# Kernel tuning notes

Hardware: AMD Instinct MI355X
Metric: run time of the kernel (lower is better)

Reference implementation:

```python
import jax, jax.numpy as jnp
import numpy as np

B, N, PAST = 2, 1024, 1024
DIM, HEADS, DH = 2048, 16, 128
INNER = HEADS * DH
LN_EPS = 1e-5
ROPE_THETA = 10000.0


def setup_inputs() -> dict:
    key = jax.random.key(0)
    k0, k1, k2, k3, k4 = jax.random.split(key, 5)
    x = jax.random.normal(k0, (B, N, DIM), dtype=jnp.float32)
    past_k = jax.random.normal(k1, (B, HEADS, PAST, DH), dtype=jnp.float32)
    past_v = jax.random.normal(k2, (B, HEADS, PAST, DH), dtype=jnp.float32)
    # causal mask with KV-cache offset: query i sits at global pos PAST+i,
    # mask (True = blocked) keys at positions j > PAST+i
    kv = PAST + N
    q_pos = PAST + jnp.arange(N)
    k_pos = jnp.arange(kv)
    mask = jnp.broadcast_to((k_pos[None, :] > q_pos[:, None])[None, None], (B, 1, N, kv))
    w_qkv = jax.random.normal(k3, (DIM, 3 * INNER), dtype=jnp.float32) * (DIM ** -0.5)
    w_out = jax.random.normal(k4, (INNER, DIM), dtype=jnp.float32) * (INNER ** -0.5)
    ln_g = jnp.ones((DIM,), dtype=jnp.float32)
    ln_b = jnp.zeros((DIM,), dtype=jnp.float32)
    return {"x": x, "past_k": past_k, "past_v": past_v, "mask": mask,
            "w_qkv": w_qkv, "w_out": w_out, "ln_g": ln_g, "ln_b": ln_b}


def _layernorm(x, g, b):
    mu = jnp.mean(x, axis=-1, keepdims=True)
    var = jnp.mean((x - mu) ** 2, axis=-1, keepdims=True)
    return (x - mu) * jax.lax.rsqrt(var + LN_EPS) * g + b


def _rope(t, pos):
    # interleaved rotary (lucidrains rotary-embedding-torch convention)
    inv_freq = 1.0 / (ROPE_THETA ** (jnp.arange(0, DH, 2, dtype=jnp.float32) / DH))
    freqs = pos.astype(jnp.float32)[:, None] * inv_freq[None, :]   # [n, DH/2]
    freqs = jnp.repeat(freqs, 2, axis=-1)                          # [n, DH]
    cos = jnp.cos(freqs).astype(t.dtype)
    sin = jnp.sin(freqs).astype(t.dtype)
    t2 = t.reshape(*t.shape[:-1], DH // 2, 2)
    rot = jnp.stack((-t2[..., 1], t2[..., 0]), axis=-1).reshape(t.shape)
    return t * cos + rot * sin


def reference(x, past_k, past_v, mask, w_qkv, w_out, ln_g, ln_b):
    b, n, _ = x.shape
    xn = _layernorm(x, ln_g, ln_b)
    qkv = xn @ w_qkv                                               # [b, n, 3*INNER]
    q, k, v = jnp.split(qkv, 3, axis=-1)
    to_heads = lambda t: t.reshape(b, n, HEADS, DH).transpose(0, 2, 1, 3)  # b h n d
    q, k, v = to_heads(q), to_heads(k), to_heads(v)
    k = jnp.concatenate((past_k, k), axis=2)                       # [b, h, kv, d]
    v = jnp.concatenate((past_v, v), axis=2)
    kv_len = k.shape[2]
    q = _rope(q, jnp.arange(n) + (kv_len - n))
    k = _rope(k, jnp.arange(kv_len))
    scale = DH ** -0.5
    dots = jnp.einsum('bhnd,bhmd->bhnm', q, k) * scale             # [b, h, n, kv]
    dots = jnp.where(mask, -jnp.inf, dots)
    attn = jax.nn.softmax(dots, axis=-1)
    out = jnp.einsum('bhnm,bhmd->bhnd', attn, v)                   # [b, h, n, d]
    out = out.transpose(0, 2, 1, 3).reshape(b, n, INNER)
    return out @ w_out, k, v
```

## Files before the change

kernel.cpp:

```cpp
#include <hip/hip_runtime.h>
#include <hip/hip_bf16.h>
#include <math.h>

#define BB    2
#define NN    1024
#define PAST  1024
#define KVL   2048
#define DIM   2048
#define HEADS 16
#define DH    128
#define INNER 2048
#define NQKV  6144
#define TOK   2048
#define LN_EPS 1e-5f

typedef __attribute__((ext_vector_type(8))) short   short8;
typedef __attribute__((ext_vector_type(4))) float   f32x4;
typedef __attribute__((ext_vector_type(8))) unsigned short us8;
typedef __attribute__((ext_vector_type(4))) unsigned short us4;
typedef unsigned short us;

__device__ __forceinline__ float bfbits2f(us u) {
    return __uint_as_float(((unsigned int)u) << 16);
}
__device__ __forceinline__ us f2bfb(float f) {
    union { __hip_bfloat16 h; us u; } cv;
    cv.h = __float2bfloat16(f);
    return cv.u;
}
__device__ __forceinline__ us8 pack8u(float4 a, float4 b) {
    us8 r;
    r[0] = f2bfb(a.x); r[1] = f2bfb(a.y); r[2] = f2bfb(a.z); r[3] = f2bfb(a.w);
    r[4] = f2bfb(b.x); r[5] = f2bfb(b.y); r[6] = f2bfb(b.z); r[7] = f2bfb(b.w);
    return r;
}

__device__ __forceinline__ void gload_lds16(const void* gsrc, void* ldst) {
    __builtin_amdgcn_global_load_lds(
        (const __attribute__((address_space(1))) void*)gsrc,
        (__attribute__((address_space(3))) void*)ldst, 16, 0, 0);
}

__global__ __launch_bounds__(256) void transp_kernel(
    const float* __restrict__ src, us* __restrict__ dst, int R, int C)
{
    const int c0 = blockIdx.x * 64;
    const int r0 = blockIdx.y * 64;
    const int tid = threadIdx.x;

    __shared__ us T[64][68];

    #pragma unroll
    for (int e = 0; e < 4; e++) {
        int idx = tid + e * 256;
        int jr  = idx >> 4;
        int c4  = (idx & 15) * 4;
        float4 v = *reinterpret_cast<const float4*>(
            src + (size_t)(r0 + jr) * C + c0 + c4);
        us4 w;
        w[0] = f2bfb(v.x); w[1] = f2bfb(v.y); w[2] = f2bfb(v.z); w[3] = f2bfb(v.w);
        *reinterpret_cast<us4*>(&T[jr][c4]) = w;
    }
    __syncthreads();

    #pragma unroll
    for (int e = 0; e < 4; e++) {
        int idx = tid + e * 256;
        int d   = idx >> 4;
        int k4  = (idx & 15) * 4;
        us4 w;
        w[0] = T[k4 + 0][d];
        w[1] = T[k4 + 1][d];
        w[2] = T[k4 + 2][d];
        w[3] = T[k4 + 3][d];
        *reinterpret_cast<us4*>(dst + (size_t)(c0 + d) * R + r0 + k4) = w;
    }
}

__global__ __launch_bounds__(256) void ln_kernel(
    const float* __restrict__ x, const float* __restrict__ g,
    const float* __restrict__ b, us* __restrict__ xn)
{
    const int t   = blockIdx.x;
    const int tid = threadIdx.x;
    const size_t base = (size_t)t * DIM;

    float4 p0 = reinterpret_cast<const float4*>(x + base)[tid * 2 + 0];
    float4 p1 = reinterpret_cast<const float4*>(x + base)[tid * 2 + 1];
    float v[8] = {p0.x, p0.y, p0.z, p0.w, p1.x, p1.y, p1.z, p1.w};

    float s1 = 0.f, s2 = 0.f;
    #pragma unroll
    for (int i = 0; i < 8; i++) { s1 += v[i]; s2 += v[i] * v[i]; }

    #pragma unroll
    for (int off = 32; off; off >>= 1) {
        s1 += __shfl_xor(s1, off);
        s2 += __shfl_xor(s2, off);
    }
    __shared__ float red1[4], red2[4];
    if ((tid & 63) == 0) { red1[tid >> 6] = s1; red2[tid >> 6] = s2; }
    __syncthreads();
    float S1 = red1[0] + red1[1] + red1[2] + red1[3];
    float S2 = red2[0] + red2[1] + red2[2] + red2[3];
    const float inv = 1.0f / (float)DIM;
    float mu  = S1 * inv;
    float var = S2 * inv - mu * mu;
    float rstd = rsqrtf(var + LN_EPS);

    const int d0 = tid * 8;
    float4 oa, ob;
    oa.x = (v[0] - mu) * rstd * g[d0 + 0] + b[d0 + 0];
    oa.y = (v[1] - mu) * rstd * g[d0 + 1] + b[d0 + 1];
    oa.z = (v[2] - mu) * rstd * g[d0 + 2] + b[d0 + 2];
    oa.w = (v[3] - mu) * rstd * g[d0 + 3] + b[d0 + 3];
    ob.x = (v[4] - mu) * rstd * g[d0 + 4] + b[d0 + 4];
    ob.y = (v[5] - mu) * rstd * g[d0 + 5] + b[d0 + 5];
    ob.z = (v[6] - mu) * rstd * g[d0 + 6] + b[d0 + 6];
    ob.w = (v[7] - mu) * rstd * g[d0 + 7] + b[d0 + 7];

    *reinterpret_cast<us8*>(xn + base + d0) = pack8u(oa, ob);
}

template<bool OUT_BF16>
__global__ __launch_bounds__(256) void gemm_bt_kernel(
    const us* __restrict__ A, const us* __restrict__ Bt,
    void* __restrict__ Cout, int M, int N, int K)
{
    __shared__ us As[2][128 * 32];
    __shared__ us Bs[2][128 * 32];

    const int tid  = threadIdx.x;
    const int wave = tid >> 6, lane = tid & 63;
    const int quad = lane >> 4, l16 = lane & 15;
    const int wm = wave & 1, wn = wave >> 1;
    const int m0 = blockIdx.y * 128, n0 = blockIdx.x * 128;

    f32x4 acc[4][4];
    #pragma unroll
    for (int i = 0; i < 4; i++)
        #pragma unroll
        for (int j = 0; j < 4; j++)
            #pragma unroll
            for (int r = 0; r < 4; r++) acc[i][j][r] = 0.f;

    const int s_row = tid >> 2;
    const int s_c8  = (tid & 3) * 8;

    auto stage = [&](int k0, int buf) {
        #pragma unroll
        for (int e = 0; e < 2; e++) {
            gload_lds16(A  + (size_t)(m0 + e * 64 + s_row) * K + k0 + s_c8,
                        (char*)&As[buf][0] + (e * 256 + tid) * 16);
            gload_lds16(Bt + (size_t)(n0 + e * 64 + s_row) * K + k0 + s_c8,
                        (char*)&Bs[buf][0] + (e * 256 + tid) * 16);
        }
    };

    stage(0, 0);
    __syncthreads();

    int buf = 0;
    for (int k0 = 0; k0 < K; k0 += 32) {
        if (k0 + 32 < K) stage(k0 + 32, buf ^ 1);

        short8 af[4], bf[4];
        #pragma unroll
        for (int mi = 0; mi < 4; mi++)
            af[mi] = *reinterpret_cast<const short8*>(
                &As[buf][(wm * 64 + mi * 16 + l16) * 32 + quad * 8]);
        #pragma unroll
        for (int ni = 0; ni < 4; ni++)
            bf[ni] = *reinterpret_cast<const short8*>(
                &Bs[buf][(wn * 64 + ni * 16 + l16) * 32 + quad * 8]);

        __builtin_amdgcn_s_setprio(1);
        #pragma unroll
        for (int mi = 0; mi < 4; mi++)
            #pragma unroll
            for (int ni = 0; ni < 4; ni++)
                acc[mi][ni] = __builtin_amdgcn_mfma_f32_16x16x32_bf16(
                    af[mi], bf[ni], acc[mi][ni], 0, 0, 0);
        __builtin_amdgcn_s_setprio(0);

        __syncthreads();
        buf ^= 1;
    }

    #pragma unroll
    for (int mi = 0; mi < 4; mi++) {
        #pragma unroll
        for (int r = 0; r < 4; r++) {
            size_t row = (size_t)(m0 + wm * 64 + mi * 16 + quad * 4 + r);
            #pragma unroll
            for (int ni = 0; ni < 4; ni++) {
                size_t col = n0 + wn * 64 + ni * 16 + l16;
                if (OUT_BF16)
                    ((us*)Cout)[row * N + col] = f2bfb(acc[mi][ni][r]);
                else
                    ((float*)Cout)[row * N + col] = acc[mi][ni][r];
            }
        }
    }
}

__global__ __launch_bounds__(256) void rope_kernel(
    const float* __restrict__ past_k, const float* __restrict__ past_v,
    us* __restrict__ qkv, float* __restrict__ out_k, float* __restrict__ out_v,
    us* __restrict__ Kbf)
{
    const int tid  = threadIdx.x;
    const int pid  = blockIdx.x * 4 + (tid >> 6);
    const int lane = tid & 63;

    const int b   = pid / (HEADS * KVL);
    const int rem = pid - b * (HEADS * KVL);
    const int h   = rem / KVL;
    const int pos = rem - h * KVL;

    const float invf = exp2f((float)lane * (-13.287712379549449f / 64.0f));
    float sn, cs;
    sincosf((float)pos * invf, &sn, &cs);

    const size_t obase = ((size_t)(b * HEADS + h) * KVL + pos) * DH + 2 * lane;

    float k0, k1;
    if (pos < PAST) {
        const size_t pbase = ((size_t)(b * HEADS + h) * PAST + pos) * DH + 2 * lane;
        k0 = past_k[pbase];
        k1 = past_k[pbase + 1];
    } else {
        const int t = b * NN + (pos - PAST);
        const us* qp = qkv + (size_t)t * NQKV + INNER + h * DH + 2 * lane;
        k0 = bfbits2f(qp[0]); k1 = bfbits2f(qp[1]);
    }
    float kr0 = k0 * cs - k1 * sn;
    float kr1 = k1 * cs + k0 * sn;
    out_k[obase]     = kr0;
    out_k[obase + 1] = kr1;
    Kbf[obase]       = f2bfb(kr0);
    Kbf[obase + 1]   = f2bfb(kr1);

    if (pos < PAST) {
        const size_t pbase = ((size_t)(b * HEADS + h) * PAST + pos) * DH + 2 * lane;
        out_v[obase]     = past_v[pbase];
        out_v[obase + 1] = past_v[pbase + 1];
    } else {
        const int t = b * NN + (pos - PAST);
        const us* vp = qkv + (size_t)t * NQKV + 2 * INNER + h * DH + 2 * lane;
        out_v[obase]     = bfbits2f(vp[0]);
        out_v[obase + 1] = bfbits2f(vp[1]);
    }

    if (pos >= PAST) {
        const int t = b * NN + (pos - PAST);
        us* qq = qkv + (size_t)t * NQKV + h * DH + 2 * lane;
        float q0 = bfbits2f(qq[0]), q1 = bfbits2f(qq[1]);
        qq[0] = f2bfb(q0 * cs - q1 * sn);
        qq[1] = f2bfb(q1 * cs + q0 * sn);
    }
}

__global__ __launch_bounds__(256) void vtrans_kernel(
    const float* __restrict__ Vc, us* __restrict__ Vtg)
{
    const int jb = blockIdx.x;
    const int db = blockIdx.y;
    const int bh = blockIdx.z;
    const int tid = threadIdx.x;

    __shared__ us T[64][68];

    const float* src = Vc + ((size_t)bh * KVL + jb * 64) * DH + db * 64;
    #pragma unroll
    for (int e = 0; e < 4; e++) {
        int idx = tid + e * 256;
        int jr  = idx >> 4;
        int c4  = (idx & 15) * 4;
        float4 v = *reinterpret_cast<const float4*>(src + (size_t)jr * DH + c4);
        us4 w;
        w[0] = f2bfb(v.x); w[1] = f2bfb(v.y); w[2] = f2bfb(v.z); w[3] = f2bfb(v.w);
        *reinterpret_cast<us4*>(&T[jr][c4]) = w;
    }
    __syncthreads();

    us* dst = Vtg + ((size_t)bh * DH + db * 64) * KVL + jb * 64;
    #pragma unroll
    for (int e = 0; e < 4; e++) {
        int idx = tid + e * 256;
        int d   = idx >> 4;
        int k4  = (idx & 15) * 4;
        us4 w;
        w[0] = T[k4 + 0][d];
        w[1] = T[k4 + 1][d];
        w[2] = T[k4 + 2][d];
        w[3] = T[k4 + 3][d];
        *reinterpret_cast<us4*>(dst + (size_t)d * KVL + k4) = w;
    }
}

__global__ __launch_bounds__(512) void attn_mfma_kernel(
    const us* __restrict__ qkv,
    const us* __restrict__ Kbf,
    const us* __restrict__ Vtg,
    us* __restrict__ Ao)
{
    const int tid  = threadIdx.x;
    const int wave = tid >> 6;
    const int lane = tid & 63;
    const int quad = lane >> 4;
    const int l16  = lane & 15;

    const int flat = blockIdx.x;
    const int s    = flat >> 3;
    const int g    = (flat & 7) + 8 * (s & 3);
    const int p    = s >> 2;
    const int h    = g & 15;
    const int b    = g >> 4;
    const int qtile = (wave < 4) ? p : (15 - p);
    const int nch   = 32 - p;
    const int mynch = (wave < 4) ? (17 + p) : (32 - p);

    __shared__ us Ks[2][64 * 128];
    __shared__ us Vt[2][128 * 64];
    __shared__ us Pb[8][16 * 64];

    short8 qf[4];
    {
        const int qrow = qtile * 64 + (wave & 3) * 16 + l16;
        const us* qp = qkv + (size_t)(b * NN + qrow) * NQKV + h * DH;
        #pragma unroll
        for (int ks = 0; ks < 4; ks++)
            qf[ks] = *reinterpret_cast<const short8*>(qp + ks * 32 + quad * 8);
    }

    f32x4 Oacc[8];
    #pragma unroll
    for (int t = 0; t < 8; t++)
        #pragma unroll
        for (int r = 0; r < 4; r++) Oacc[t][r] = 0.f;
    float m_run  = -INFINITY;
    float l_part = 0.f;

    const us* kptr = Kbf + (size_t)(b * HEADS + h) * KVL * DH;
    const us* vtb  = Vtg + (size_t)(b * HEADS + h) * DH * KVL;
    const float scale = 0.08838834764831845f;
    const float THRU  = 90.50966799f;
    const int qg  = PAST + qtile * 64 + (wave & 3) * 16 + l16;
    const int swz = (l16 & 7) << 4;
    char* pbb = (char*)&Pb[wave][0];

    auto stage = [&](int j0, int buf) {
        #pragma unroll
        for (int e = 0; e < 2; e++) {
            int phys = (e * 512 + tid) * 16;
            int row  = phys >> 8;
            int col  = (phys & 255) ^ ((row & 7) << 4);
            gload_lds16((const char*)(kptr + (size_t)(j0 + row) * DH) + col,
                        (char*)&Ks[buf][0] + phys);
        }
        #pragma unroll
        for (int e = 0; e < 2; e++) {
            int phys = (e * 512 + tid) * 16;
            int row  = phys >> 7;
            int col  = (phys & 127) ^ ((row & 7) << 4);
            gload_lds16((const char*)(vtb + (size_t)row * KVL) + j0 * 2 + col,
                        (char*)&Vt[buf][0] + phys);
        }
    };

    stage(0, 0);
    __syncthreads();

    int cur = 0;
    for (int c = 0; c < nch; c++) {
        const int j0 = c * 64;
        if (c + 1 < nch) stage(j0 + 64, cur ^ 1);

        if (c < mynch) {
            f32x4 S[4];
            #pragma unroll
            for (int t = 0; t < 4; t++)
                #pragma unroll
                for (int r = 0; r < 4; r++) S[t][r] = 0.f;
            __builtin_amdgcn_s_setprio(1);
            #pragma unroll
            for (int ks = 0; ks < 4; ks++) {
                #pragma unroll
                for (int t = 0; t < 4; t++) {
                    int row  = t * 16 + l16;
                    int colb = ks * 64 + quad * 16;
                    const char* kp = (const char*)&Ks[cur][0] +
                                    row * 256 + (colb ^ ((row & 7) << 4));
                    short8 kb = *reinterpret_cast<const short8*>(kp);
                    S[t] = __builtin_amdgcn_mfma_f32_16x16x32_bf16(kb, qf[ks], S[t], 0, 0, 0);
                }
            }
            __builtin_amdgcn_s_setprio(0);

            const int rel = qg - j0;
            float mx = -INFINITY;
            #pragma unroll
            for (int t = 0; t < 4; t++) {
                #pragma unroll
                for (int r = 0; r < 4; r++) {
                    int koff = t * 16 + quad * 4 + r;
                    S[t][r] = (koff <= rel) ? S[t][r] : -INFINITY;
                    mx = fmaxf(mx, S[t][r]);
                }
            }
            mx = fmaxf(mx, __shfl_xor(mx, 16));
            mx = fmaxf(mx, __shfl_xor(mx, 32));

            float alpha = 1.f;
            if (__any(mx > m_run + THRU)) {
                float nm = fmaxf(m_run, mx);
                alpha = __expf((m_run - nm) * scale);
                m_run = nm;
                float al[4];
                #pragma unroll
                for (int r = 0; r < 4; r++) al[r] = __shfl(alpha, quad * 4 + r);
                #pragma unroll
                for (int t2 = 0; t2 < 8; t2++) {
                    Oacc[t2][0] *= al[0]; Oacc[t2][1] *= al[1];
                    Oacc[t2][2] *= al[2]; Oacc[t2][3] *= al[3];
                }
            }

            const float nmk = -m_run * scale;
            float rs = 0.f;
            #pragma unroll
            for (int t = 0; t < 4; t++) {
                us4 w;
                #pragma unroll
                for (int r = 0; r < 4; r++) {
                    float pv = __expf(fmaf(S[t][r], scale, nmk));
                    rs += pv;
                    w[r] = f2bfb(pv);
                }
                *reinterpret_cast<us4*>(pbb + l16 * 128 +
                                        ((t * 32 + quad * 8) ^ swz)) = w;
            }
            l_part = l_part * alpha + rs;

            asm volatile("s_waitcnt lgkmcnt(0)" ::: "memory");
            __builtin_amdgcn_sched_barrier(0);

            __builtin_amdgcn_s_setprio(1);
            #pragma unroll
            for (int kh = 0; kh < 2; kh++) {
                short8 pa = *reinterpret_cast<const short8*>(
                    pbb + l16 * 128 + ((kh * 64 + quad * 16) ^ swz));
                #pragma unroll
                for (int t2 = 0; t2 < 8; t2++) {
                    int row  = t2 * 16 + l16;
                    int colb = kh * 64 + quad * 16;
                    const char* vp = (const char*)&Vt[cur][0] +
                                    row * 128 + (colb ^ ((row & 7) << 4));
                    short8 vb = *reinterpret_cast<const short8*>(vp);
                    Oacc[t2] = __builtin_amdgcn_mfma_f32_16x16x32_bf16(pa, vb, Oacc[t2], 0, 0, 0);
                }
            }
            __builtin_amdgcn_s_setprio(0);
        }

        __syncthreads();
        cur ^= 1;
    }

    l_part += __shfl_xor(l_part, 16);
    l_part += __shfl_xor(l_part, 32);
    float invl[4];
    #pragma unroll
    for (int r = 0; r < 4; r++)
        invl[r] = 1.f / __shfl(l_part, quad * 4 + r);

    const int row0 = b * NN + qtile * 64 + (wave & 3) * 16 + quad * 4;
    #pragma unroll
    for (int r = 0; r < 4; r++) {
        us* dst = Ao + (size_t)(row0 + r) * INNER + h * DH + l16;
        #pragma unroll
        for (int t2 = 0; t2 < 8; t2++)
            dst[t2 * 16] = f2bfb(Oacc[t2][r] * invl[r]);
    }
}

extern "C" void kernel_launch(void* const* d_in, const int* in_sizes, int n_in,
                              void* d_out, int out_size, void* d_ws, size_t ws_size,
                              hipStream_t stream)
{
    const float* x      = (const float*)d_in[0];
    const float* past_k = (const float*)d_in[1];
    const float* past_v = (const float*)d_in[2];
    const float* w_qkv  = (const float*)d_in[4];
    const float* w_out  = (const float*)d_in[5];
    const float* ln_g   = (const float*)d_in[6];
    const float* ln_b   = (const float*)d_in[7];

    float* out   = (float*)d_out;
    float* out_k = out   + (size_t)BB * NN * DIM;
    float* out_v = out_k + (size_t)BB * HEADS * KVL * DH;

    us* xn   = (us*)d_ws;
    us* qkv  = xn  + (size_t)TOK * DIM;
    us* Wqt  = qkv + (size_t)TOK * NQKV;
    us* Wot  = Wqt + (size_t)NQKV * DIM;
    us* Vtg  = Wot + (size_t)DIM * INNER;
    us* attn = xn;
    us* Kbf  = Wqt;

    transp_kernel<<<dim3(NQKV / 64, DIM / 64), 256, 0, stream>>>(
        w_qkv, Wqt, DIM, NQKV);
    transp_kernel<<<dim3(DIM / 64, INNER / 64), 256, 0, stream>>>(
        w_out, Wot, INNER, DIM);

    ln_kernel<<<TOK, 256, 0, stream>>>(x, ln_g, ln_b, xn);

    gemm_bt_kernel<true><<<dim3(NQKV / 128, TOK / 128), 256, 0, stream>>>(
        xn, Wqt, (void*)qkv, TOK, NQKV, DIM);

    rope_kernel<<<(BB * HEADS * KVL) / 4, 256, 0, stream>>>(
        past_k, past_v, qkv, out_k, out_v, Kbf);

    vtrans_kernel<<<dim3(KVL / 64, DH / 64, BB * HEADS), 256, 0, stream>>>(
        out_v, Vtg);

    attn_mfma_kernel<<<256, 512, 0, stream>>>(
        qkv, Kbf, Vtg, attn);

    gemm_bt_kernel<false><<<dim3(DIM / 128, TOK / 128), 256, 0, stream>>>(
        attn, Wot, (void*)out, TOK, DIM, INNER);
}
```

Baseline: 378.7 us.

## Switch attention to 32x32 MFMA with in-register P, triple-buffer GEMM and attention

The attention kernel moves from 16x16x32 to 32x32x16 bf16 MFMA with 4 waves of 32 query rows each. The softmax probabilities are repacked in registers via v_permlane32_swap instead of a round trip through shared memory. Both the GEMM and the attention kernel go from double to triple buffering with explicit vmcnt waits in place of __syncthreads, and the GEMM LDS layout is XOR-swizzled to cut bank conflicts. The goal is fewer LDS round trips and more load/compute overlap, at the cost of more LDS per block and fewer waves per attention block, which may hurt occupancy.

```diff
diff --git a/kernel.cpp b/kernel.cpp
--- a/kernel.cpp
+++ b/kernel.cpp
@@ -14,10 +14,11 @@
 #define TOK   2048
 #define LN_EPS 1e-5f
 
-typedef __attribute__((ext_vector_type(8))) short   short8;
-typedef __attribute__((ext_vector_type(4))) float   f32x4;
-typedef __attribute__((ext_vector_type(8))) unsigned short us8;
-typedef __attribute__((ext_vector_type(4))) unsigned short us4;
+typedef __attribute__((ext_vector_type(8)))  short    short8;
+typedef __attribute__((ext_vector_type(4)))  float    f32x4;
+typedef __attribute__((ext_vector_type(16))) float    f32x16;
+typedef __attribute__((ext_vector_type(8)))  unsigned short us8;
+typedef __attribute__((ext_vector_type(4)))  unsigned short us4;
 typedef unsigned short us;
 
 __device__ __forceinline__ float bfbits2f(us u) {
@@ -27,6 +28,9 @@
     union { __hip_bfloat16 h; us u; } cv;
     cv.h = __float2bfloat16(f);
     return cv.u;
+}
+__device__ __forceinline__ unsigned pkbf(float a, float b) {
+    return (unsigned)f2bfb(a) | ((unsigned)f2bfb(b) << 16);
 }
 __device__ __forceinline__ us8 pack8u(float4 a, float4 b) {
     us8 r;
@@ -127,8 +131,8 @@
     const us* __restrict__ A, const us* __restrict__ Bt,
     void* __restrict__ Cout, int M, int N, int K)
 {
-    __shared__ us As[2][128 * 32];
-    __shared__ us Bs[2][128 * 32];
+    __shared__ us As[3][128 * 32];
+    __shared__ us Bs[3][128 * 32];
 
     const int tid  = threadIdx.x;
     const int wave = tid >> 6, lane = tid & 63;
@@ -144,35 +148,50 @@
             #pragma unroll
             for (int r = 0; r < 4; r++) acc[i][j][r] = 0.f;
 
-    const int s_row = tid >> 2;
-    const int s_c8  = (tid & 3) * 8;
-
     auto stage = [&](int k0, int buf) {
         #pragma unroll
         for (int e = 0; e < 2; e++) {
-            gload_lds16(A  + (size_t)(m0 + e * 64 + s_row) * K + k0 + s_c8,
-                        (char*)&As[buf][0] + (e * 256 + tid) * 16);
-            gload_lds16(Bt + (size_t)(n0 + e * 64 + s_row) * K + k0 + s_c8,
-                        (char*)&Bs[buf][0] + (e * 256 + tid) * 16);
+            int phys = (e * 256 + tid) * 16;
+            int lr   = phys >> 7;
+            int offp = (phys & 127) ^ ((lr & 7) << 4);
+            int m    = 2 * lr + (offp >> 6);
+            int kb   = offp & 63;
+            gload_lds16((const char*)(A + (size_t)(m0 + m) * K + k0) + kb,
+                        (char*)&As[buf][0] + phys);
+            gload_lds16((const char*)(Bt + (size_t)(n0 + m) * K + k0) + kb,
+                        (char*)&Bs[buf][0] + phys);
         }
     };
 
+    const int ns = K >> 5;
     stage(0, 0);
-    __syncthreads();
-
-    int buf = 0;
-    for (int k0 = 0; k0 < K; k0 += 32) {
-        if (k0 + 32 < K) stage(k0 + 32, buf ^ 1);
+    stage(32, 1);
+    __builtin_amdgcn_sched_barrier(0);
+    asm volatile("s_waitcnt vmcnt(4)" ::: "memory");
+    __builtin_amdgcn_s_barrier();
+    __builtin_amdgcn_sched_barrier(0);
+
+    int cur = 0;
+    for (int ks = 0; ks < ns; ks++) {
+        if (ks + 2 < ns) stage((ks + 2) * 32, (ks + 2) % 3);
 
         short8 af[4], bf[4];
         #pragma unroll
-        for (int mi = 0; mi < 4; mi++)
+        for (int mi = 0; mi < 4; mi++) {
+            int mrow = wm * 64 + mi * 16 + l16;
+            int lr   = mrow >> 1;
+            int off  = ((mrow & 1) * 64 + quad * 16) ^ ((lr & 7) << 4);
             af[mi] = *reinterpret_cast<const short8*>(
-                &As[buf][(wm * 64 + mi * 16 + l16) * 32 + quad * 8]);
-        #pragma unroll
-        for (int ni = 0; ni < 4; ni++)
+                (const char*)&As[cur][0] + lr * 128 + off);
+        }
+        #pragma unroll
+        for (int ni = 0; ni < 4; ni++) {
+            int nrow = wn * 64 + ni * 16 + l16;
+            int lr   = nrow >> 1;
+            int off  = ((nrow & 1) * 64 + quad * 16) ^ ((lr & 7) << 4);
             bf[ni] = *reinterpret_cast<const short8*>(
-                &Bs[buf][(wn * 64 + ni * 16 + l16) * 32 + quad * 8]);
+                (const char*)&Bs[cur][0] + lr * 128 + off);
+        }
 
         __builtin_amdgcn_s_setprio(1);
         #pragma unroll
@@ -183,8 +202,12 @@
                     af[mi], bf[ni], acc[mi][ni], 0, 0, 0);
         __builtin_amdgcn_s_setprio(0);
 
-        __syncthreads();
-        buf ^= 1;
+        __builtin_amdgcn_sched_barrier(0);
+        if (ks + 2 < ns) asm volatile("s_waitcnt vmcnt(4)" ::: "memory");
+        else             asm volatile("s_waitcnt vmcnt(0)" ::: "memory");
+        __builtin_amdgcn_s_barrier();
+        __builtin_amdgcn_sched_barrier(0);
+        cur = (cur == 2) ? 0 : cur + 1;
     }
 
     #pragma unroll
@@ -299,7 +322,7 @@
     }
 }
 
-__global__ __launch_bounds__(512) void attn_mfma_kernel(
+__global__ __launch_bounds__(256) void attn_mfma_kernel(
     const us* __restrict__ qkv,
     const us* __restrict__ Kbf,
     const us* __restrict__ Vtg,
@@ -308,37 +331,37 @@
     const int tid  = threadIdx.x;
     const int wave = tid >> 6;
     const int lane = tid & 63;
-    const int quad = lane >> 4;
-    const int l16  = lane & 15;
+    const int l32  = lane & 31;
+    const int g    = lane >> 5;
 
     const int flat = blockIdx.x;
     const int s    = flat >> 3;
-    const int g    = (flat & 7) + 8 * (s & 3);
+    const int grp  = (flat & 7) + 8 * (s & 3);
     const int p    = s >> 2;
-    const int h    = g & 15;
-    const int b    = g >> 4;
-    const int qtile = (wave < 4) ? p : (15 - p);
+    const int h    = grp & 15;
+    const int b    = grp >> 4;
+    const int qtile = (wave < 2) ? p : (15 - p);
+    const int qsub  = (wave & 1) * 32;
+    const int mynch = 17 + qtile;
     const int nch   = 32 - p;
-    const int mynch = (wave < 4) ? (17 + p) : (32 - p);
-
-    __shared__ us Ks[2][64 * 128];
-    __shared__ us Vt[2][128 * 64];
-    __shared__ us Pb[8][16 * 64];
-
-    short8 qf[4];
+
+    __shared__ us Ks[3][64 * 128];
+    __shared__ us Vt[3][128 * 64];
+
+    short8 qf[8];
     {
-        const int qrow = qtile * 64 + (wave & 3) * 16 + l16;
+        const int qrow = qtile * 64 + qsub + l32;
         const us* qp = qkv + (size_t)(b * NN + qrow) * NQKV + h * DH;
         #pragma unroll
-        for (int ks = 0; ks < 4; ks++)
-            qf[ks] = *reinterpret_cast<const short8*>(qp + ks * 32 + quad * 8);
-    }
-
-    f32x4 Oacc[8];
-    #pragma unroll
-    for (int t = 0; t < 8; t++)
-        #pragma unroll
-        for (int r = 0; r < 4; r++) Oacc[t][r] = 0.f;
+        for (int ks = 0; ks < 8; ks++)
+            qf[ks] = *reinterpret_cast<const short8*>(qp + ks * 16 + g * 8);
+    }
+
+    f32x16 Oacc[4];
+    #pragma unroll
+    for (int dt = 0; dt < 4; dt++)
+        #pragma unroll
+        for (int r = 0; r < 16; r++) Oacc[dt][r] = 0.f;
     float m_run  = -INFINITY;
     float l_part = 0.f;
 
@@ -346,22 +369,20 @@
     const us* vtb  = Vtg + (size_t)(b * HEADS + h) * DH * KVL;
     const float scale = 0.08838834764831845f;
     const float THRU  = 90.50966799f;
-    const int qg  = PAST + qtile * 64 + (wave & 3) * 16 + l16;
-    const int swz = (l16 & 7) << 4;
-    char* pbb = (char*)&Pb[wave][0];
+    const int qg = PAST + qtile * 64 + qsub + l32;
 
     auto stage = [&](int j0, int buf) {
         #pragma unroll
-        for (int e = 0; e < 2; e++) {
-            int phys = (e * 512 + tid) * 16;
+        for (int e = 0; e < 4; e++) {
+            int phys = (e * 256 + tid) * 16;
             int row  = phys >> 8;
             int col  = (phys & 255) ^ ((row & 7) << 4);
             gload_lds16((const char*)(kptr + (size_t)(j0 + row) * DH) + col,
                         (char*)&Ks[buf][0] + phys);
         }
         #pragma unroll
-        for (int e = 0; e < 2; e++) {
-            int phys = (e * 512 + tid) * 16;
+        for (int e = 0; e < 4; e++) {
+            int phys = (e * 256 + tid) * 16;
             int row  = phys >> 7;
             int col  = (phys & 127) ^ ((row & 7) << 4);
             gload_lds16((const char*)(vtb + (size_t)row * KVL) + j0 * 2 + col,
@@ -370,30 +391,36 @@
     };
 
     stage(0, 0);
-    __syncthreads();
+    stage(64, 1);
+    __builtin_amdgcn_sched_barrier(0);
+    asm volatile("s_waitcnt vmcnt(8)" ::: "memory");
+    __builtin_amdgcn_s_barrier();
+    __builtin_amdgcn_sched_barrier(0);
 
     int cur = 0;
     for (int c = 0; c < nch; c++) {
         const int j0 = c * 64;
-        if (c + 1 < nch) stage(j0 + 64, cur ^ 1);
+        if (c + 2 < nch) stage(j0 + 128, (c + 2) % 3 == 0 ? 0 : ((c + 2) % 3));
 
         if (c < mynch) {
-            f32x4 S[4];
-            #pragma unroll
-            for (int t = 0; t < 4; t++)
-                #pragma unroll
-                for (int r = 0; r < 4; r++) S[t][r] = 0.f;
+            f32x16 S[2];
+            #pragma unroll
+            for (int t = 0; t < 2; t++)
+                #pragma unroll
+                for (int r = 0; r < 16; r++) S[t][r] = 0.f;
+
             __builtin_amdgcn_s_setprio(1);
             #pragma unroll
-            for (int ks = 0; ks < 4; ks++) {
-                #pragma unroll
-                for (int t = 0; t < 4; t++) {
-                    int row  = t * 16 + l16;
-                    int colb = ks * 64 + quad * 16;
+            for (int ks = 0; ks < 8; ks++) {
+                #pragma unroll
+                for (int t = 0; t < 2; t++) {
+                    int row  = t * 32 + l32;
+                    int colb = ks * 32 + g * 16;
                     const char* kp = (const char*)&Ks[cur][0] +
-                                    row * 256 + (colb ^ ((row & 7) << 4));
+                                     row * 256 + (colb ^ ((row & 7) << 4));
                     short8 kb = *reinterpret_cast<const short8*>(kp);
-                    S[t] = __builtin_amdgcn_mfma_f32_16x16x32_bf16(kb, qf[ks], S[t], 0, 0, 0);
+                    S[t] = __builtin_amdgcn_mfma_f32_32x32x16_bf16(
+                        kb, qf[ks], S[t], 0, 0, 0);
                 }
             }
             __builtin_amdgcn_s_setprio(0);
@@ -401,15 +428,13 @@
             const int rel = qg - j0;
             float mx = -INFINITY;
             #pragma unroll
-            for (int t = 0; t < 4; t++) {
-                #pragma unroll
-                for (int r = 0; r < 4; r++) {
-                    int koff = t * 16 + quad * 4 + r;
-                    S[t][r] = (koff <= rel) ? S[t][r] : -INFINITY;
+            for (int t = 0; t < 2; t++)
+                #pragma unroll
+                for (int r = 0; r < 16; r++) {
+                    int kvo = t * 32 + (r & 3) + 8 * (r >> 2) + 4 * g;
+                    S[t][r] = (kvo <= rel) ? S[t][r] : -INFINITY;
                     mx = fmaxf(mx, S[t][r]);
                 }
-            }
-            mx = fmaxf(mx, __shfl_xor(mx, 16));
             mx = fmaxf(mx, __shfl_xor(mx, 32));
 
             float alpha = 1.f;
@@ -417,71 +442,80 @@
                 float nm = fmaxf(m_run, mx);
                 alpha = __expf((m_run - nm) * scale);
                 m_run = nm;
-                float al[4];
-                #pragma unroll
-                for (int r = 0; r < 4; r++) al[r] = __shfl(alpha, quad * 4 + r);
-                #pragma unroll
-                for (int t2 = 0; t2 < 8; t2++) {
-                    Oacc[t2][0] *= al[0]; Oacc[t2][1] *= al[1];
-                    Oacc[t2][2] *= al[2]; Oacc[t2][3] *= al[3];
+                #pragma unroll
+                for (int r = 0; r < 16; r++) {
+                    float ar = __shfl(alpha, (r & 3) + 8 * (r >> 2) + 4 * g);
+                    Oacc[0][r] *= ar; Oacc[1][r] *= ar;
+                    Oacc[2][r] *= ar; Oacc[3][r] *= ar;
                 }
             }
 
             const float nmk = -m_run * scale;
             float rs = 0.f;
             #pragma unroll
-            for (int t = 0; t < 4; t++) {
-                us4 w;
-                #pragma unroll
-                for (int r = 0; r < 4; r++) {
+            for (int t = 0; t < 2; t++)
+                #pragma unroll
+                for (int r = 0; r < 16; r++) {
                     float pv = __expf(fmaf(S[t][r], scale, nmk));
+                    S[t][r] = pv;
                     rs += pv;
-                    w[r] = f2bfb(pv);
                 }
-                *reinterpret_cast<us4*>(pbb + l16 * 128 +
-                                        ((t * 32 + quad * 8) ^ swz)) = w;
-            }
             l_part = l_part * alpha + rs;
 
-            asm volatile("s_waitcnt lgkmcnt(0)" ::: "memory");
-            __builtin_amdgcn_sched_barrier(0);
+            short8 paf[4];
+            #pragma unroll
+            for (int t = 0; t < 2; t++)
+                #pragma unroll
+                for (int u = 0; u < 2; u++) {
+                    unsigned cA = pkbf(S[t][8*u + 0], S[t][8*u + 1]);
+                    unsigned cB = pkbf(S[t][8*u + 2], S[t][8*u + 3]);
+                    unsigned dA = pkbf(S[t][8*u + 4], S[t][8*u + 5]);
+                    unsigned dB = pkbf(S[t][8*u + 6], S[t][8*u + 7]);
+                    asm volatile("v_permlane32_swap_b32 %0, %1"
+                                 : "+v"(cA), "+v"(dA));
+                    asm volatile("v_permlane32_swap_b32 %0, %1"
+                                 : "+v"(cB), "+v"(dB));
+                    union { unsigned u4[4]; short8 s8; } fb;
+                    fb.u4[0] = cA; fb.u4[1] = cB; fb.u4[2] = dA; fb.u4[3] = dB;
+                    paf[t * 2 + u] = fb.s8;
+                }
 
             __builtin_amdgcn_s_setprio(1);
             #pragma unroll
-            for (int kh = 0; kh < 2; kh++) {
-                short8 pa = *reinterpret_cast<const short8*>(
-                    pbb + l16 * 128 + ((kh * 64 + quad * 16) ^ swz));
-                #pragma unroll
-                for (int t2 = 0; t2 < 8; t2++) {
-                    int row  = t2 * 16 + l16;
-                    int colb = kh * 64 + quad * 16;
+            for (int ks = 0; ks < 4; ks++) {
+                #pragma unroll
+                for (int dt = 0; dt < 4; dt++) {
+                    int row  = dt * 32 + l32;
+                    int colb = ks * 32 + g * 16;
                     const char* vp = (const char*)&Vt[cur][0] +
-                                    row * 128 + (colb ^ ((row & 7) << 4));
+                                     row * 128 + (colb ^ ((row & 7) << 4));
                     short8 vb = *reinterpret_cast<const short8*>(vp);
-                    Oacc[t2] = __builtin_amdgcn_mfma_f32_16x16x32_bf16(pa, vb, Oacc[t2], 0, 0, 0);
+                    Oacc[dt] = __builtin_amdgcn_mfma_f32_32x32x16_bf16(
+                        paf[ks], vb, Oacc[dt], 0, 0, 0);
                 }
             }
             __builtin_amdgcn_s_setprio(0);
         }
 
-        __syncthreads();
-        cur ^= 1;
-    }
-
-    l_part += __shfl_xor(l_part, 16);
+        __builtin_amdgcn_sched_barrier(0);
+        if (c + 2 < nch) asm volatile("s_waitcnt vmcnt(8)" ::: "memory");
+        else             asm volatile("s_waitcnt vmcnt(0)" ::: "memory");
+        __builtin_amdgcn_s_barrier();
+        __builtin_amdgcn_sched_barrier(0);
+        cur = (cur == 2) ? 0 : cur + 1;
+    }
+
     l_part += __shfl_xor(l_part, 32);
-    float invl[4];
-    #pragma unroll
-    for (int r = 0; r < 4; r++)
-        invl[r] = 1.f / __shfl(l_part, quad * 4 + r);
-
-    const int row0 = b * NN + qtile * 64 + (wave & 3) * 16 + quad * 4;
-    #pragma unroll
-    for (int r = 0; r < 4; r++) {
-        us* dst = Ao + (size_t)(row0 + r) * INNER + h * DH + l16;
-        #pragma unroll
-        for (int t2 = 0; t2 < 8; t2++)
-            dst[t2 * 16] = f2bfb(Oacc[t2][r] * invl[r]);
+    float linv = 1.f / l_part;
+    #pragma unroll
+    for (int r = 0; r < 16; r++) {
+        int qr = (r & 3) + 8 * (r >> 2) + 4 * g;
+        float iv = __shfl(linv, qr);
+        int qrow = qtile * 64 + qsub + qr;
+        us* dst = Ao + (size_t)(b * NN + qrow) * INNER + h * DH + l32;
+        #pragma unroll
+        for (int dt = 0; dt < 4; dt++)
+            dst[dt * 32] = f2bfb(Oacc[dt][r] * iv);
     }
 }
 
@@ -525,7 +559,7 @@
     vtrans_kernel<<<dim3(KVL / 64, DH / 64, BB * HEADS), 256, 0, stream>>>(
         out_v, Vtg);
 
-    attn_mfma_kernel<<<256, 512, 0, stream>>>(
+    attn_mfma_kernel<<<256, 256, 0, stream>>>(
         qkv, Kbf, Vtg, attn);
 
     gemm_bt_kernel<false><<<dim3(DIM / 128, TOK / 128), 256, 0, stream>>>(
```

Measured after the change: 392.6 us. 1.04x slower.
